# Kernel tuning notes

Measured on AMD Instinct MI355X. Metric: run time of the kernel, lower is better.

## Reference

```python
import jax, jax.numpy as jnp
import numpy as np

B, T, E, H = 2, 2048, 1024, 4
Dk = E // H          # 256 head qk dim
Dv = Dk * 2          # 512 head v dim (expansion_ratio=2)
EPS = 1e-5
ROPE_BASE = 10000.0


def setup_inputs() -> dict:
    key = jax.random.key(0)
    ks = jax.random.split(key, 7)
    s = 0.02  # small init matching xavier gains in reset_parameters
    return {
        "x": jax.random.normal(ks[0], (B, T, E), jnp.float32),
        "Wq": jax.random.normal(ks[1], (E, E), jnp.float32) * s,
        "Wk": jax.random.normal(ks[2], (E, E), jnp.float32) * s,
        "Wv": jax.random.normal(ks[3], (E, 2 * E), jnp.float32) * s,
        "Wg": jax.random.normal(ks[4], (E, 2 * E), jnp.float32) * s,
        "Wo": jax.random.normal(ks[5], (2 * E, E), jnp.float32) * s,
        "gn_weight": jnp.ones((Dv,), jnp.float32),
    }


def _rotary(q, k):
    # q,k: [b, t, h, d]; non-interleaved (GPT-NeoX) rotary over the full head dim
    d = q.shape[-1]
    inv_freq = 1.0 / (ROPE_BASE ** (jnp.arange(0, d, 2, dtype=jnp.float32) / d))
    t = jnp.arange(q.shape[1], dtype=jnp.float32)
    freqs = jnp.einsum('t,f->tf', t, inv_freq)      # [t, d/2]
    cos = jnp.cos(freqs)[None, :, None, :]
    sin = jnp.sin(freqs)[None, :, None, :]

    def rot(x):
        x1, x2 = x[..., : d // 2], x[..., d // 2:]
        return jnp.concatenate([x1 * cos - x2 * sin, x2 * cos + x1 * sin], axis=-1)

    return rot(q), rot(k)


def reference(x, Wq, Wk, Wv, Wg, Wo, gn_weight):
    b, t, e = x.shape
    q = (x @ Wq).reshape(b, t, H, Dk)
    k = (x @ Wk).reshape(b, t, H, Dk)
    q, k = _rotary(q, k)
    q = q.transpose(0, 2, 1, 3) * (Dk ** -0.5)      # [b,h,t,dk], scale = head_qk_dim^-0.5
    k = k.transpose(0, 2, 1, 3)
    v = (x @ Wv).reshape(b, t, H, Dv).transpose(0, 2, 1, 3)  # [b,h,t,dv]

    # RetNet per-head decay: gamma_h = 1 - 2^-(5+h)
    gamma = 1.0 - jnp.exp2(-5.0 - jnp.arange(H, dtype=jnp.float32))
    ti = jnp.arange(t)
    n = ti[:, None] - ti[None, :]                   # t - s
    decay = jnp.where(
        n >= 0,
        gamma[:, None, None] ** jnp.maximum(n, 0).astype(jnp.float32),
        0.0,
    )                                               # [h,t,t] causal decayed mask

    scores = jnp.einsum('bhtd,bhsd->bhts', q, k) * decay[None]
    o = jnp.einsum('bhts,bhsd->bhtd', scores, v)    # [b,h,t,dv]
    o = o.transpose(0, 2, 1, 3)                     # [b,t,h,dv]

    # per-head RMSNorm (group_norm over head_v_dim)
    rms = jnp.sqrt(jnp.mean(o * o, axis=-1, keepdims=True) + EPS)
    o = o / rms * gn_weight

    # NOTE: the given source multiplies by raw g_proj(x) (gate_fn not applied in forward)
    g = x @ Wg                                      # [b,t,2E]
    return (o.reshape(b, t, H * Dv) * g) @ Wo       # [b,t,E]
```

## Files before the change

kernel.cpp:

```cpp
#include <hip/hip_runtime.h>
#include <hip/hip_bf16.h>

#define B_ 2
#define T_ 2048
#define E_ 1024
#define DK 256
#define DV 512
#define MROWS 4096
#define LDQKVG 6144
#define LDOG 2048

typedef __attribute__((ext_vector_type(8))) short short8;
typedef __attribute__((ext_vector_type(4))) float floatx4;

typedef __attribute__((address_space(3))) unsigned as3_u32;
typedef const __attribute__((address_space(1))) unsigned as1_u32;

static __device__ __forceinline__ void gld_lds16(const unsigned short* gsrc, unsigned short* ldst) {
  __builtin_amdgcn_global_load_lds((as1_u32*)gsrc, (as3_u32*)ldst, 16, 0, 0);
}

static __device__ __forceinline__ float bf2f(unsigned short u) {
  union { unsigned int i; float f; } x; x.i = ((unsigned int)u) << 16; return x.f;
}
static __device__ __forceinline__ unsigned short f2bf(float f) {
  __hip_bfloat16 h = __float2bfloat16(f);
  return __builtin_bit_cast(unsigned short, h);
}
static __device__ __forceinline__ float load_as_f(const float* p) { return *p; }
static __device__ __forceinline__ float load_as_f(const unsigned short* p) { return bf2f(*p); }

__global__ void __launch_bounds__(256) convx_kernel(const float* __restrict__ x,
                                                    unsigned short* __restrict__ xb) {
  int i = blockIdx.x * 256 + threadIdx.x;
  size_t base = (size_t)i * 8;
  float4 a = *(const float4*)(x + base);
  float4 b = *(const float4*)(x + base + 4);
  short8 o;
  o[0] = (short)f2bf(a.x); o[1] = (short)f2bf(a.y);
  o[2] = (short)f2bf(a.z); o[3] = (short)f2bf(a.w);
  o[4] = (short)f2bf(b.x); o[5] = (short)f2bf(b.y);
  o[6] = (short)f2bf(b.z); o[7] = (short)f2bf(b.w);
  *(short8*)(xb + base) = o;
}

template<typename TIN>
__global__ void __launch_bounds__(256) transpose_bf16_kernel(
    const TIN* __restrict__ in, int ldin, unsigned short* __restrict__ out, int ldout) {
  __shared__ float tile[32][33];
  int c0 = blockIdx.x * 32, r0 = blockIdx.y * 32;
  int tx = threadIdx.x & 31, ty = threadIdx.x >> 5;
#pragma unroll
  for (int i = 0; i < 32; i += 8)
    tile[ty + i][tx] = load_as_f(&in[(size_t)(r0 + ty + i) * ldin + c0 + tx]);
  __syncthreads();
#pragma unroll
  for (int i = 0; i < 32; i += 8)
    out[(size_t)(c0 + ty + i) * ldout + r0 + tx] = f2bf(tile[tx][ty + i]);
}

template<bool F32OUT>
__global__ void __launch_bounds__(256) gemm_bt_kernel(
    const unsigned short* __restrict__ A, const unsigned short* __restrict__ Bt,
    void* __restrict__ Cp, int K, int ldc, int ccol0) {
  __shared__ unsigned short As[128 * 32];
  __shared__ unsigned short Bs[128 * 32];
  const int tid = threadIdx.x;
  const int lane = tid & 63;
  const int wid = tid >> 6;
  const int m0 = blockIdx.x * 128;
  const int n0 = blockIdx.y * 128;
  const int wr = (wid >> 1) * 64, wc = (wid & 1) * 64;
  floatx4 acc[4][4];
#pragma unroll
  for (int i = 0; i < 4; i++)
#pragma unroll
    for (int j = 0; j < 4; j++)
      acc[i][j] = (floatx4){0.f, 0.f, 0.f, 0.f};

  for (int k0 = 0; k0 < K; k0 += 32) {
    __syncthreads();
#pragma unroll
    for (int j = 0; j < 2; ++j) {
      int ci = (wid * 2 + j) * 64 + lane;
      int row = ci >> 2, cc = (ci & 3) * 8;
      gld_lds16(&A[(size_t)(m0 + row) * K + k0 + cc], &As[(wid * 2 + j) * 64 * 8]);
      gld_lds16(&Bt[(size_t)(n0 + row) * K + k0 + cc], &Bs[(wid * 2 + j) * 64 * 8]);
    }
    __syncthreads();
    short8 af[4], bfr[4];
#pragma unroll
    for (int mb = 0; mb < 4; mb++)
      af[mb] = *(const short8*)&As[(wr + mb * 16 + (lane & 15)) * 32 + (lane >> 4) * 8];
#pragma unroll
    for (int nb = 0; nb < 4; nb++)
      bfr[nb] = *(const short8*)&Bs[(wc + nb * 16 + (lane & 15)) * 32 + (lane >> 4) * 8];
#pragma unroll
    for (int mb = 0; mb < 4; mb++)
#pragma unroll
      for (int nb = 0; nb < 4; nb++)
        acc[mb][nb] = __builtin_amdgcn_mfma_f32_16x16x32_bf16(af[mb], bfr[nb], acc[mb][nb], 0, 0, 0);
  }
#pragma unroll
  for (int mb = 0; mb < 4; mb++)
#pragma unroll
    for (int nb = 0; nb < 4; nb++)
#pragma unroll
      for (int r = 0; r < 4; r++) {
        int row = m0 + wr + mb * 16 + (lane >> 4) * 4 + r;
        int col = ccol0 + n0 + wc + nb * 16 + (lane & 15);
        float v = acc[mb][nb][r];
        if (F32OUT) ((float*)Cp)[(size_t)row * ldc + col] = v;
        else ((unsigned short*)Cp)[(size_t)row * ldc + col] = f2bf(v);
      }
}

__global__ void __launch_bounds__(256) rope_kernel(unsigned short* __restrict__ qkvg) {
  int idx = blockIdx.x * 256 + threadIdx.x;
  int j = idx & 127;
  int h = (idx >> 7) & 3;
  int row = idx >> 9;
  int t = row & (T_ - 1);
  float invf = exp2f(-(float)j * (13.287712379549449f / 128.0f));
  float ang = (float)t * invf;
  float c = cosf(ang), s = sinf(ang);
  size_t base = (size_t)row * LDQKVG + h * DK + j;
  float q1 = bf2f(qkvg[base]), q2 = bf2f(qkvg[base + 128]);
  float k1 = bf2f(qkvg[base + E_]), k2 = bf2f(qkvg[base + E_ + 128]);
  qkvg[base]            = f2bf((q1 * c - q2 * s) * 0.0625f);
  qkvg[base + 128]      = f2bf((q2 * c + q1 * s) * 0.0625f);
  qkvg[base + E_]       = f2bf(k1 * c - k2 * s);
  qkvg[base + E_ + 128] = f2bf(k2 * c + k1 * s);
}

__global__ void __launch_bounds__(256) retention_kernel(
    const unsigned short* __restrict__ qkvg, const unsigned short* __restrict__ vT,
    const float* __restrict__ gnw, unsigned short* __restrict__ og) {
  __shared__ unsigned short k_lds[2][32 * 256];
  __shared__ unsigned short v_lds[2][512 * 32];
  __shared__ unsigned short s_lds[2][16 * 32];
  __shared__ float rms_lds[32][2];
  const int tid = threadIdx.x, lane = tid & 63, wid = tid >> 6;
  const int rh = wid & 1, dh = wid >> 1;
  const int bh = blockIdx.x & 7, p = blockIdx.x >> 3;
  const int b = bh >> 2, h = bh & 3;
  const float log2g = log2f(1.0f - exp2f(-5.0f - (float)h));
  const unsigned short* kbase = qkvg + (size_t)b * T_ * LDQKVG + E_ + h * DK;
  const unsigned short* vbase = vT + (size_t)h * DV * MROWS + b * T_;

  auto stage = [&](int buf, int sb) {
    int s0 = sb * 32;
#pragma unroll
    for (int j = 0; j < 4; ++j) {
      int ci = (wid * 4 + j) * 64 + lane;
      int row = ci >> 5, c = ci & 31;
      int cs = c ^ (row & 7);
      gld_lds16(kbase + (size_t)(s0 + row) * LDQKVG + cs * 8,
                &k_lds[buf][(wid * 4 + j) * 64 * 8]);
    }
#pragma unroll
    for (int j = 0; j < 8; ++j) {
      int ci = (wid * 8 + j) * 64 + lane;
      int dv = ci >> 2, c = ci & 3;
      int cs = c ^ ((dv ^ (dv >> 2)) & 3);
      gld_lds16(vbase + (size_t)dv * MROWS + s0 + cs * 8,
                &v_lds[buf][(wid * 8 + j) * 64 * 8]);
    }
  };

#pragma unroll 1
  for (int half = 0; half < 2; ++half) {
    const int tt = half == 0 ? p : 63 - p;
    const int r0 = tt * 32;
    const int nsb = tt + 1;

    short8 qf[8];
    {
      int qrow = b * T_ + r0 + rh * 16 + (lane & 15);
      const unsigned short* qp = qkvg + (size_t)qrow * LDQKVG + h * DK + (lane >> 4) * 8;
#pragma unroll
      for (int kk = 0; kk < 8; kk++) qf[kk] = *(const short8*)(qp + kk * 32);
    }
    floatx4 oacc[16];
#pragma unroll
    for (int i = 0; i < 16; i++) oacc[i] = (floatx4){0.f, 0.f, 0.f, 0.f};

    stage(0, 0);
#pragma unroll 1
    for (int sb = 0; sb < nsb; ++sb) {
      const int cur = sb & 1;
      __syncthreads();
      floatx4 f = (floatx4){0.f, 0.f, 0.f, 0.f};
      const int scol_l = dh * 16 + (lane & 15);
#pragma unroll
      for (int kk = 0; kk < 8; kk++) {
        int c = (kk * 4 + (lane >> 4)) ^ (scol_l & 7);
        short8 kf = *(const short8*)&k_lds[cur][scol_l * 256 + c * 8];
        f = __builtin_amdgcn_mfma_f32_16x16x32_bf16(qf[kk], kf, f, 0, 0, 0);
      }
      const int s0 = sb * 32;
#pragma unroll
      for (int r = 0; r < 4; ++r) {
        int lr = (lane >> 4) * 4 + r;
        int qrow_h = r0 + rh * 16 + lr;
        int scol = s0 + dh * 16 + (lane & 15);
        int n = qrow_h - scol;
        float val = (n >= 0) ? f[r] * exp2f((float)n * log2g) : 0.0f;
        int cc = dh * 16 + (lane & 15);
        int byte = lr * 64 + ((cc * 2) ^ ((lr & 3) << 4));
        *(unsigned short*)((char*)s_lds[rh] + byte) = f2bf(val);
      }
      __syncthreads();
      if (sb + 1 < nsb) stage(cur ^ 1, sb + 1);
      short8 af;
      {
        int row = lane & 15;
        int byte = row * 64 + (((lane >> 4) * 16) ^ ((row & 3) << 4));
        af = *(const short8*)((char*)s_lds[rh] + byte);
      }
#pragma unroll
      for (int nb = 0; nb < 16; ++nb) {
        int dv = dh * 256 + nb * 16 + (lane & 15);
        int c = (lane >> 4) ^ ((dv ^ (dv >> 2)) & 3);
        short8 vf = *(const short8*)&v_lds[cur][dv * 32 + c * 8];
        oacc[nb] = __builtin_amdgcn_mfma_f32_16x16x32_bf16(af, vf, oacc[nb], 0, 0, 0);
      }
    }
    float ssp[4];
#pragma unroll
    for (int r = 0; r < 4; ++r) {
      float ss = 0.f;
#pragma unroll
      for (int nb = 0; nb < 16; nb++) { float xv = oacc[nb][r]; ss += xv * xv; }
      ss += __shfl_xor(ss, 1, 64);
      ss += __shfl_xor(ss, 2, 64);
      ss += __shfl_xor(ss, 4, 64);
      ss += __shfl_xor(ss, 8, 64);
      ssp[r] = ss;
    }
    if ((lane & 15) == 0) {
#pragma unroll
      for (int r = 0; r < 4; ++r)
        rms_lds[rh * 16 + (lane >> 4) * 4 + r][dh] = ssp[r];
    }
    __syncthreads();
#pragma unroll
    for (int r = 0; r < 4; ++r) {
      int lrow = rh * 16 + (lane >> 4) * 4 + r;
      float tot = rms_lds[lrow][0] + rms_lds[lrow][1];
      float inv = rsqrtf(tot * (1.0f / 512.0f) + 1e-5f);
      int qrow = b * T_ + r0 + rh * 16 + (lane >> 4) * 4 + r;
      size_t growbase = (size_t)qrow * LDQKVG + 4096 + h * DV + dh * 256;
      size_t orowbase = (size_t)qrow * LDOG + h * DV + dh * 256;
#pragma unroll
      for (int nb = 0; nb < 16; nb++) {
        int col = nb * 16 + (lane & 15);
        float gv = bf2f(qkvg[growbase + col]);
        og[orowbase + col] = f2bf(oacc[nb][r] * inv * gnw[dh * 256 + col] * gv);
      }
    }
    __syncthreads();
  }
}

extern "C" void kernel_launch(void* const* d_in, const int* in_sizes, int n_in,
                              void* d_out, int out_size, void* d_ws, size_t ws_size,
                              hipStream_t stream) {
  const float* x   = (const float*)d_in[0];
  const float* Wq  = (const float*)d_in[1];
  const float* Wk  = (const float*)d_in[2];
  const float* Wv  = (const float*)d_in[3];
  const float* Wg  = (const float*)d_in[4];
  const float* Wo  = (const float*)d_in[5];
  const float* gnw = (const float*)d_in[6];
  float* out = (float*)d_out;

  char* ws = (char*)d_ws;
  size_t off = 0;
  auto alloc = [&](size_t bytes) { char* p = ws + off; off += (bytes + 255) & ~(size_t)255; return p; };
  unsigned short* xb    = (unsigned short*)alloc((size_t)MROWS * E_ * 2);
  unsigned short* WallT = (unsigned short*)alloc((size_t)6144 * 1024 * 2);
  unsigned short* WoT   = (unsigned short*)alloc((size_t)1024 * 2048 * 2);
  unsigned short* qkvg  = (unsigned short*)alloc((size_t)MROWS * LDQKVG * 2);
  unsigned short* vT    = (unsigned short*)alloc((size_t)2048 * MROWS * 2);
  unsigned short* og    = (unsigned short*)alloc((size_t)MROWS * LDOG * 2);

  convx_kernel<<<2048, 256, 0, stream>>>(x, xb);

  transpose_bf16_kernel<float><<<dim3(32, 32), 256, 0, stream>>>(Wq, 1024, WallT, 1024);
  transpose_bf16_kernel<float><<<dim3(32, 32), 256, 0, stream>>>(Wk, 1024, WallT + (size_t)1024 * 1024, 1024);
  transpose_bf16_kernel<float><<<dim3(64, 32), 256, 0, stream>>>(Wv, 2048, WallT + (size_t)2048 * 1024, 1024);
  transpose_bf16_kernel<float><<<dim3(64, 32), 256, 0, stream>>>(Wg, 2048, WallT + (size_t)4096 * 1024, 1024);
  transpose_bf16_kernel<float><<<dim3(32, 64), 256, 0, stream>>>(Wo, 1024, WoT, 2048);

  gemm_bt_kernel<false><<<dim3(32, 48), 256, 0, stream>>>(xb, WallT, qkvg, 1024, LDQKVG, 0);

  rope_kernel<<<8192, 256, 0, stream>>>(qkvg);

  transpose_bf16_kernel<unsigned short><<<dim3(64, 128), 256, 0, stream>>>(qkvg + 2048, LDQKVG, vT, MROWS);

  retention_kernel<<<256, 256, 0, stream>>>(qkvg, vT, gnw, og);

  gemm_bt_kernel<true><<<dim3(32, 8), 256, 0, stream>>>(og, WoT, out, 2048, E_, 0);
}
```

Before: 258.4 us.

## Split retention over value-dim halves, defer RMS norm, shrink output GEMM M-tile

```diff
diff --git a/kernel.cpp b/kernel.cpp
--- a/kernel.cpp
+++ b/kernel.cpp
@@ -59,50 +59,57 @@
     out[(size_t)(c0 + ty + i) * ldout + r0 + tx] = f2bf(tile[tx][ty + i]);
 }
 
-template<bool F32OUT>
+template<int MTILE, bool F32OUT>
 __global__ void __launch_bounds__(256) gemm_bt_kernel(
     const unsigned short* __restrict__ A, const unsigned short* __restrict__ Bt,
     void* __restrict__ Cp, int K, int ldc, int ccol0) {
-  __shared__ unsigned short As[128 * 32];
+  __shared__ unsigned short As[MTILE * 32];
   __shared__ unsigned short Bs[128 * 32];
+  constexpr int MB = MTILE / 32;
+  constexpr int AJ = MTILE / 64;
   const int tid = threadIdx.x;
   const int lane = tid & 63;
   const int wid = tid >> 6;
-  const int m0 = blockIdx.x * 128;
+  const int m0 = blockIdx.x * MTILE;
   const int n0 = blockIdx.y * 128;
-  const int wr = (wid >> 1) * 64, wc = (wid & 1) * 64;
-  floatx4 acc[4][4];
-#pragma unroll
-  for (int i = 0; i < 4; i++)
+  const int wr = (wid >> 1) * (MTILE / 2), wc = (wid & 1) * 64;
+  floatx4 acc[MB][4];
+#pragma unroll
+  for (int i = 0; i < MB; i++)
 #pragma unroll
     for (int j = 0; j < 4; j++)
       acc[i][j] = (floatx4){0.f, 0.f, 0.f, 0.f};
 
   for (int k0 = 0; k0 < K; k0 += 32) {
     __syncthreads();
+#pragma unroll
+    for (int j = 0; j < AJ; ++j) {
+      int ci = (wid * AJ + j) * 64 + lane;
+      int row = ci >> 2, cc = (ci & 3) * 8;
+      gld_lds16(&A[(size_t)(m0 + row) * K + k0 + cc], &As[(wid * AJ + j) * 512]);
+    }
 #pragma unroll
     for (int j = 0; j < 2; ++j) {
       int ci = (wid * 2 + j) * 64 + lane;
       int row = ci >> 2, cc = (ci & 3) * 8;
-      gld_lds16(&A[(size_t)(m0 + row) * K + k0 + cc], &As[(wid * 2 + j) * 64 * 8]);
-      gld_lds16(&Bt[(size_t)(n0 + row) * K + k0 + cc], &Bs[(wid * 2 + j) * 64 * 8]);
+      gld_lds16(&Bt[(size_t)(n0 + row) * K + k0 + cc], &Bs[(wid * 2 + j) * 512]);
     }
     __syncthreads();
-    short8 af[4], bfr[4];
-#pragma unroll
-    for (int mb = 0; mb < 4; mb++)
+    short8 af[MB], bfr[4];
+#pragma unroll
+    for (int mb = 0; mb < MB; mb++)
       af[mb] = *(const short8*)&As[(wr + mb * 16 + (lane & 15)) * 32 + (lane >> 4) * 8];
 #pragma unroll
     for (int nb = 0; nb < 4; nb++)
       bfr[nb] = *(const short8*)&Bs[(wc + nb * 16 + (lane & 15)) * 32 + (lane >> 4) * 8];
 #pragma unroll
-    for (int mb = 0; mb < 4; mb++)
+    for (int mb = 0; mb < MB; mb++)
 #pragma unroll
       for (int nb = 0; nb < 4; nb++)
         acc[mb][nb] = __builtin_amdgcn_mfma_f32_16x16x32_bf16(af[mb], bfr[nb], acc[mb][nb], 0, 0, 0);
   }
 #pragma unroll
-  for (int mb = 0; mb < 4; mb++)
+  for (int mb = 0; mb < MB; mb++)
 #pragma unroll
     for (int nb = 0; nb < 4; nb++)
 #pragma unroll
@@ -135,18 +142,19 @@
 
 __global__ void __launch_bounds__(256) retention_kernel(
     const unsigned short* __restrict__ qkvg, const unsigned short* __restrict__ vT,
-    const float* __restrict__ gnw, unsigned short* __restrict__ og) {
+    const float* __restrict__ gnw, unsigned short* __restrict__ og,
+    float* __restrict__ ssbuf) {
   __shared__ unsigned short k_lds[2][32 * 256];
-  __shared__ unsigned short v_lds[2][512 * 32];
-  __shared__ unsigned short s_lds[2][16 * 32];
+  __shared__ unsigned short v_lds[2][256 * 32];
+  __shared__ unsigned short s_lds[2][16 * 40];
   __shared__ float rms_lds[32][2];
   const int tid = threadIdx.x, lane = tid & 63, wid = tid >> 6;
   const int rh = wid & 1, dh = wid >> 1;
-  const int bh = blockIdx.x & 7, p = blockIdx.x >> 3;
+  const int bh = blockIdx.x & 7, dvh = (blockIdx.x >> 3) & 1, p = blockIdx.x >> 4;
   const int b = bh >> 2, h = bh & 3;
   const float log2g = log2f(1.0f - exp2f(-5.0f - (float)h));
   const unsigned short* kbase = qkvg + (size_t)b * T_ * LDQKVG + E_ + h * DK;
-  const unsigned short* vbase = vT + (size_t)h * DV * MROWS + b * T_;
+  const unsigned short* vbase = vT + (size_t)(h * DV + dvh * 256) * MROWS + b * T_;
 
   auto stage = [&](int buf, int sb) {
     int s0 = sb * 32;
@@ -155,16 +163,14 @@
       int ci = (wid * 4 + j) * 64 + lane;
       int row = ci >> 5, c = ci & 31;
       int cs = c ^ (row & 7);
-      gld_lds16(kbase + (size_t)(s0 + row) * LDQKVG + cs * 8,
-                &k_lds[buf][(wid * 4 + j) * 64 * 8]);
-    }
-#pragma unroll
-    for (int j = 0; j < 8; ++j) {
-      int ci = (wid * 8 + j) * 64 + lane;
+      gld_lds16(kbase + (size_t)(s0 + row) * LDQKVG + cs * 8, &k_lds[buf][(wid * 4 + j) * 512]);
+    }
+#pragma unroll
+    for (int j = 0; j < 4; ++j) {
+      int ci = (wid * 4 + j) * 64 + lane;
       int dv = ci >> 2, c = ci & 3;
       int cs = c ^ ((dv ^ (dv >> 2)) & 3);
-      gld_lds16(vbase + (size_t)dv * MROWS + s0 + cs * 8,
-                &v_lds[buf][(wid * 8 + j) * 64 * 8]);
+      gld_lds16(vbase + (size_t)dv * MROWS + s0 + cs * 8, &v_lds[buf][(wid * 4 + j) * 512]);
     }
   };
 
@@ -181,9 +187,9 @@
 #pragma unroll
       for (int kk = 0; kk < 8; kk++) qf[kk] = *(const short8*)(qp + kk * 32);
     }
-    floatx4 oacc[16];
-#pragma unroll
-    for (int i = 0; i < 16; i++) oacc[i] = (floatx4){0.f, 0.f, 0.f, 0.f};
+    floatx4 oacc[8];
+#pragma unroll
+    for (int i = 0; i < 8; i++) oacc[i] = (floatx4){0.f, 0.f, 0.f, 0.f};
 
     stage(0, 0);
 #pragma unroll 1
@@ -206,61 +212,68 @@
         int scol = s0 + dh * 16 + (lane & 15);
         int n = qrow_h - scol;
         float val = (n >= 0) ? f[r] * exp2f((float)n * log2g) : 0.0f;
-        int cc = dh * 16 + (lane & 15);
-        int byte = lr * 64 + ((cc * 2) ^ ((lr & 3) << 4));
-        *(unsigned short*)((char*)s_lds[rh] + byte) = f2bf(val);
+        s_lds[rh][lr * 40 + dh * 16 + (lane & 15)] = f2bf(val);
       }
       __syncthreads();
       if (sb + 1 < nsb) stage(cur ^ 1, sb + 1);
-      short8 af;
-      {
-        int row = lane & 15;
-        int byte = row * 64 + (((lane >> 4) * 16) ^ ((row & 3) << 4));
-        af = *(const short8*)((char*)s_lds[rh] + byte);
-      }
-#pragma unroll
-      for (int nb = 0; nb < 16; ++nb) {
-        int dv = dh * 256 + nb * 16 + (lane & 15);
+      short8 af = *(const short8*)&s_lds[rh][(lane & 15) * 40 + (lane >> 4) * 8];
+#pragma unroll
+      for (int nb = 0; nb < 8; ++nb) {
+        int dv = dh * 128 + nb * 16 + (lane & 15);
         int c = (lane >> 4) ^ ((dv ^ (dv >> 2)) & 3);
         short8 vf = *(const short8*)&v_lds[cur][dv * 32 + c * 8];
         oacc[nb] = __builtin_amdgcn_mfma_f32_16x16x32_bf16(af, vf, oacc[nb], 0, 0, 0);
       }
     }
-    float ssp[4];
 #pragma unroll
     for (int r = 0; r < 4; ++r) {
       float ss = 0.f;
 #pragma unroll
-      for (int nb = 0; nb < 16; nb++) { float xv = oacc[nb][r]; ss += xv * xv; }
+      for (int nb = 0; nb < 8; nb++) { float xv = oacc[nb][r]; ss += xv * xv; }
       ss += __shfl_xor(ss, 1, 64);
       ss += __shfl_xor(ss, 2, 64);
       ss += __shfl_xor(ss, 4, 64);
       ss += __shfl_xor(ss, 8, 64);
-      ssp[r] = ss;
-    }
-    if ((lane & 15) == 0) {
-#pragma unroll
-      for (int r = 0; r < 4; ++r)
-        rms_lds[rh * 16 + (lane >> 4) * 4 + r][dh] = ssp[r];
+      if ((lane & 15) == 0) rms_lds[rh * 16 + (lane >> 4) * 4 + r][dh] = ss;
     }
     __syncthreads();
+    if (dh == 0 && (lane & 15) == 0) {
+#pragma unroll
+      for (int r = 0; r < 4; ++r) {
+        int rl = rh * 16 + (lane >> 4) * 4 + r;
+        ssbuf[(size_t)(b * T_ + r0 + rl) * 8 + h * 2 + dvh] = rms_lds[rl][0] + rms_lds[rl][1];
+      }
+    }
 #pragma unroll
     for (int r = 0; r < 4; ++r) {
-      int lrow = rh * 16 + (lane >> 4) * 4 + r;
-      float tot = rms_lds[lrow][0] + rms_lds[lrow][1];
-      float inv = rsqrtf(tot * (1.0f / 512.0f) + 1e-5f);
-      int qrow = b * T_ + r0 + rh * 16 + (lane >> 4) * 4 + r;
-      size_t growbase = (size_t)qrow * LDQKVG + 4096 + h * DV + dh * 256;
-      size_t orowbase = (size_t)qrow * LDOG + h * DV + dh * 256;
-#pragma unroll
-      for (int nb = 0; nb < 16; nb++) {
+      int rl = rh * 16 + (lane >> 4) * 4 + r;
+      int qrow = b * T_ + r0 + rl;
+      size_t growbase = (size_t)qrow * LDQKVG + 4096 + h * DV + dvh * 256 + dh * 128;
+      size_t orowbase = (size_t)qrow * LDOG + h * DV + dvh * 256 + dh * 128;
+#pragma unroll
+      for (int nb = 0; nb < 8; nb++) {
         int col = nb * 16 + (lane & 15);
         float gv = bf2f(qkvg[growbase + col]);
-        og[orowbase + col] = f2bf(oacc[nb][r] * inv * gnw[dh * 256 + col] * gv);
+        og[orowbase + col] = f2bf(oacc[nb][r] * gnw[dvh * 256 + dh * 128 + col] * gv);
       }
     }
     __syncthreads();
   }
+}
+
+__global__ void __launch_bounds__(256) normalize_kernel(
+    unsigned short* __restrict__ og, const float* __restrict__ ssbuf) {
+  int i = blockIdx.x * 256 + threadIdx.x;
+  size_t e0 = (size_t)i * 8;
+  int row = (int)(e0 >> 11);
+  int col = (int)(e0 & 2047);
+  int h = col >> 9;
+  float ss = ssbuf[(size_t)row * 8 + h * 2] + ssbuf[(size_t)row * 8 + h * 2 + 1];
+  float inv = rsqrtf(ss * (1.0f / 512.0f) + 1e-5f);
+  short8 v = *(const short8*)(og + e0);
+#pragma unroll
+  for (int j = 0; j < 8; j++) v[j] = (short)f2bf(bf2f((unsigned short)v[j]) * inv);
+  *(short8*)(og + e0) = v;
 }
 
 extern "C" void kernel_launch(void* const* d_in, const int* in_sizes, int n_in,
@@ -284,6 +297,7 @@
   unsigned short* qkvg  = (unsigned short*)alloc((size_t)MROWS * LDQKVG * 2);
   unsigned short* vT    = (unsigned short*)alloc((size_t)2048 * MROWS * 2);
   unsigned short* og    = (unsigned short*)alloc((size_t)MROWS * LDOG * 2);
+  float*          ssbuf = (float*)alloc((size_t)MROWS * 8 * 4);
 
   convx_kernel<<<2048, 256, 0, stream>>>(x, xb);
 
@@ -293,13 +307,15 @@
   transpose_bf16_kernel<float><<<dim3(64, 32), 256, 0, stream>>>(Wg, 2048, WallT + (size_t)4096 * 1024, 1024);
   transpose_bf16_kernel<float><<<dim3(32, 64), 256, 0, stream>>>(Wo, 1024, WoT, 2048);
 
-  gemm_bt_kernel<false><<<dim3(32, 48), 256, 0, stream>>>(xb, WallT, qkvg, 1024, LDQKVG, 0);
+  gemm_bt_kernel<128, false><<<dim3(32, 48), 256, 0, stream>>>(xb, WallT, qkvg, 1024, LDQKVG, 0);
 
   rope_kernel<<<8192, 256, 0, stream>>>(qkvg);
 
   transpose_bf16_kernel<unsigned short><<<dim3(64, 128), 256, 0, stream>>>(qkvg + 2048, LDQKVG, vT, MROWS);
 
-  retention_kernel<<<256, 256, 0, stream>>>(qkvg, vT, gnw, og);
-
-  gemm_bt_kernel<true><<<dim3(32, 8), 256, 0, stream>>>(og, WoT, out, 2048, E_, 0);
-}
+  retention_kernel<<<512, 256, 0, stream>>>(qkvg, vT, gnw, og, ssbuf);
+
+  normalize_kernel<<<4096, 256, 0, stream>>>(og, ssbuf);
+
+  gemm_bt_kernel<64, true><<<dim3(64, 8), 256, 0, stream>>>(og, WoT, out, 2048, E_, 0);
+}
```

Result: faster. 240.7 us (-6.8%).
